# Performance work log

Measured on AMD Instinct MI355X. Metric: run time of the kernel, lower is better.

The kernel has to match this reference:

```python
import jax, jax.numpy as jnp
import numpy as np

B, S, E = 4, 2048, 1024
H = 16
HD = E // H  # head_dim = 64


def setup_inputs() -> dict:
    key = jax.random.key(0)
    ks = jax.random.split(key, 12)
    sc = 0.02
    return {
        "q_encodings": jax.random.normal(ks[0], (B, S, E), jnp.float32),
        "k_encodings": jax.random.normal(ks[1], (B, S, E), jnp.float32),
        "v_encodings": jax.random.normal(ks[2], (B, S, E), jnp.float32),
        # per-head q/k/v linear weights [H, HD, HD] and biases [H, HD]
        "Wq": jax.random.normal(ks[3], (H, HD, HD), jnp.float32) * sc,
        "bq": jax.random.normal(ks[4], (H, HD), jnp.float32) * sc,
        "Wk": jax.random.normal(ks[5], (H, HD, HD), jnp.float32) * sc,
        "bk": jax.random.normal(ks[6], (H, HD), jnp.float32) * sc,
        "Wv": jax.random.normal(ks[7], (H, HD, HD), jnp.float32) * sc,
        "bv": jax.random.normal(ks[8], (H, HD), jnp.float32) * sc,
        # output projection [E, E] + bias [E]
        "Wp": jax.random.normal(ks[9], (E, E), jnp.float32) * sc,
        "bp": jax.random.normal(ks[10], (E,), jnp.float32) * sc,
        "mask": 1,
    }


def reference(q_encodings, k_encodings, v_encodings, Wq, bq, Wk, bk, Wv, bv, Wp, bp, mask):
    b, s, e = q_encodings.shape
    h, hd, _ = Wq.shape
    split = lambda x: x.reshape(b, s, h, hd)  # per-head slices of n_embd
    # batched per-head linear projections (original loops over heads)
    Q = jnp.einsum('bshd,hde->bshe', split(q_encodings), Wq) + bq
    K = jnp.einsum('bshd,hde->bshe', split(k_encodings), Wk) + bk
    V = jnp.einsum('bshd,hde->bshe', split(v_encodings), Wv) + bv
    # scaled dot-product scores [B,H,S,S]; scale uses head_dim (Attention.n_embd)
    scores = jnp.einsum('bqhd,bkhd->bhqk', Q, K) / jnp.sqrt(jnp.float32(hd))
    if mask:  # static Python flag, matches torch `if mask:`
        causal = jnp.tril(jnp.ones((s, s), jnp.float32))
        scores = scores + jnp.where(causal == 0, jnp.float32(-jnp.inf), jnp.float32(0.0))
    attn = jax.nn.softmax(scores, axis=-1)
    ctx = jnp.einsum('bhqk,bkhd->bqhd', attn, V).reshape(b, s, e)
    return ctx @ Wp + bp
```

## Files before the change

kernel.cpp:

```cpp
#include <hip/hip_runtime.h>
#include <hip/hip_bf16.h>
#include <math.h>

typedef __bf16 bf16;
typedef __bf16 bf16x8 __attribute__((ext_vector_type(8)));
typedef float f32x4 __attribute__((ext_vector_type(4)));
typedef unsigned int u32x2 __attribute__((ext_vector_type(2)));

constexpr int B = 4, S = 2048, E = 1024, H = 16, HD = 64;

constexpr float QSCALE = 0.125f * 1.44269504088896340736f;
constexpr float DTHR = 11.5f;

static __device__ __forceinline__ float exp2_fast(float x) {
#if __has_builtin(__builtin_amdgcn_exp2f)
    return __builtin_amdgcn_exp2f(x);
#else
    float r; asm("v_exp_f32 %0, %1" : "=v"(r) : "v"(x)); return r;
#endif
}

static __device__ __forceinline__ unsigned pk_bf16(float a, float b) {
    union { bf16 h[2]; unsigned u; } r;
    r.h[0] = (bf16)a; r.h[1] = (bf16)b;
    return r.u;
}

static __device__ __forceinline__ void gl16(const void* g, void* l) {
    __builtin_amdgcn_global_load_lds(
        (__attribute__((address_space(1))) void*)g,
        (__attribute__((address_space(3))) void*)l,
        16, 0, 0);
}

__global__ __launch_bounds__(256) void prep_weights(
    const float* __restrict__ Wq, const float* __restrict__ Wk,
    const float* __restrict__ Wv, const float* __restrict__ Wp,
    bf16* __restrict__ Wt, bf16* __restrict__ Wpt)
{
    __shared__ float t[64][65];
    const int tid = threadIdx.x;
    const int x = blockIdx.x, y = blockIdx.y;
    if (y < 3) {
        const int h = x, p = y;
        const float* W = (p == 0) ? Wq : (p == 1) ? Wk : Wv;
        const float scale = (p == 0) ? QSCALE : 1.0f;
        #pragma unroll
        for (int i = 0; i < 16; ++i) {
            int idx = tid + i * 256;
            int d = idx >> 6, e = idx & 63;
            t[d][e] = W[(size_t)h * 4096 + d * 64 + e];
        }
        __syncthreads();
        bf16* dst = Wt + ((size_t)p * H + h) * 4096;
        #pragma unroll
        for (int i = 0; i < 16; ++i) {
            int idx = tid + i * 256;
            int e = idx >> 6, d = idx & 63;
            dst[e * 64 + d] = (bf16)(t[d][e] * scale);
        }
    } else {
        const int k0 = (y - 3) * 64, n0 = x * 64;
        #pragma unroll
        for (int i = 0; i < 16; ++i) {
            int idx = tid + i * 256;
            int r = idx >> 6, c = idx & 63;
            t[r][c] = Wp[(size_t)(k0 + r) * E + n0 + c];
        }
        __syncthreads();
        #pragma unroll
        for (int i = 0; i < 16; ++i) {
            int idx = tid + i * 256;
            int r = idx >> 6, c = idx & 63;
            Wpt[(size_t)(n0 + r) * E + k0 + c] = (bf16)t[c][r];
        }
    }
}

__global__ __launch_bounds__(256) void qkv_proj(
    const float* __restrict__ xq, const float* __restrict__ xk, const float* __restrict__ xv,
    const bf16* __restrict__ Wt,
    const float* __restrict__ bq, const float* __restrict__ bk, const float* __restrict__ bv,
    bf16* __restrict__ Qb, bf16* __restrict__ Kb, bf16* __restrict__ Vt)
{
    const int b = blockIdx.z, h = blockIdx.y, s0 = blockIdx.x * 128;
    const int tid = threadIdx.x;
    const int w = tid >> 6, l = tid & 63;
    const int l16 = l & 15, lg = l >> 4;
    const size_t bh = (size_t)b * H + h;

    __shared__ __align__(16) bf16 xs[128][64];
    __shared__ __align__(16) bf16 Wl[64][64];
    __shared__ __align__(16) bf16 ts[10240];

    for (int p = 0; p < 3; ++p) {
        const float* x    = (p == 0) ? xq : (p == 1) ? xk : xv;
        const float* bias = (p == 0) ? bq : (p == 1) ? bk : bv;
        const float  bsc  = (p == 0) ? QSCALE : 1.0f;

        __syncthreads();
        #pragma unroll
        for (int i = 0; i < 4; ++i) {
            int idx = tid + i * 256;
            int r = idx >> 3, g = idx & 7;
            const float* src = &x[((size_t)b * S + s0 + r) * E + h * 64 + g * 8];
            float4 f0 = *(const float4*)src;
            float4 f1 = *(const float4*)(src + 4);
            union { bf16 h8[8]; uint4 u; } pk;
            pk.h8[0] = (bf16)f0.x; pk.h8[1] = (bf16)f0.y;
            pk.h8[2] = (bf16)f0.z; pk.h8[3] = (bf16)f0.w;
            pk.h8[4] = (bf16)f1.x; pk.h8[5] = (bf16)f1.y;
            pk.h8[6] = (bf16)f1.z; pk.h8[7] = (bf16)f1.w;
            *(uint4*)&xs[r][(g ^ (r & 7)) * 8] = pk.u;
        }
        const bf16* wsrc = Wt + ((size_t)p * H + h) * 4096;
        #pragma unroll
        for (int i = 0; i < 2; ++i) {
            int idx = tid + i * 256;
            int e = idx >> 3, g = idx & 7;
            *(uint4*)&Wl[e][(g ^ (e & 7)) * 8] = *(const uint4*)(wsrc + e * 64 + g * 8);
        }
        __syncthreads();

        if (p < 2) {
            float bcol[4];
            #pragma unroll
            for (int ei = 0; ei < 4; ++ei)
                bcol[ei] = bias[h * 64 + ei * 16 + l16] * bsc;
            #pragma unroll
            for (int st = 0; st < 2; ++st) {
                const int srow = w * 32 + st * 16 + l16;
                bf16x8 a0 = *(const bf16x8*)&xs[srow][((lg    ) ^ (srow & 7)) * 8];
                bf16x8 a1 = *(const bf16x8*)&xs[srow][((4 + lg) ^ (srow & 7)) * 8];
                #pragma unroll
                for (int ei = 0; ei < 4; ++ei) {
                    const int erow = ei * 16 + l16;
                    bf16x8 b0 = *(const bf16x8*)&Wl[erow][((lg    ) ^ (erow & 7)) * 8];
                    bf16x8 b1 = *(const bf16x8*)&Wl[erow][((4 + lg) ^ (erow & 7)) * 8];
                    f32x4 acc = {0.f, 0.f, 0.f, 0.f};
                    acc = __builtin_amdgcn_mfma_f32_16x16x32_bf16(a0, b0, acc, 0, 0, 0);
                    acc = __builtin_amdgcn_mfma_f32_16x16x32_bf16(a1, b1, acc, 0, 0, 0);
                    #pragma unroll
                    for (int r = 0; r < 4; ++r)
                        ts[(w * 32 + st * 16 + 4 * lg + r) * 80 + ei * 16 + l16] =
                            (bf16)(acc[r] + bcol[ei]);
                }
            }
            __syncthreads();
            bf16* out = (p == 0) ? Qb : Kb;
            #pragma unroll
            for (int i = 0; i < 4; ++i) {
                int idx = tid + i * 256;
                int r = idx >> 3, g = idx & 7;
                uint4 v = *(const uint4*)&ts[r * 80 + g * 8];
                *(uint4*)(out + (bh * S + s0 + r) * 64 + g * 8) = v;
            }
        } else {
            float brow[4];
            #pragma unroll
            for (int r = 0; r < 4; ++r)
                brow[r] = bias[h * 64 + w * 16 + 4 * lg + r];
            const int erow = w * 16 + l16;
            bf16x8 a0 = *(const bf16x8*)&Wl[erow][((lg    ) ^ (erow & 7)) * 8];
            bf16x8 a1 = *(const bf16x8*)&Wl[erow][((4 + lg) ^ (erow & 7)) * 8];
            #pragma unroll
            for (int st = 0; st < 8; ++st) {
                const int srow = st * 16 + l16;
                bf16x8 b0 = *(const bf16x8*)&xs[srow][((lg    ) ^ (srow & 7)) * 8];
                bf16x8 b1 = *(const bf16x8*)&xs[srow][((4 + lg) ^ (srow & 7)) * 8];
                f32x4 acc = {0.f, 0.f, 0.f, 0.f};
                acc = __builtin_amdgcn_mfma_f32_16x16x32_bf16(a0, b0, acc, 0, 0, 0);
                acc = __builtin_amdgcn_mfma_f32_16x16x32_bf16(a1, b1, acc, 0, 0, 0);
                #pragma unroll
                for (int r = 0; r < 4; ++r)
                    ts[(w * 16 + 4 * lg + r) * 136 + st * 16 + l16] =
                        (bf16)(acc[r] + brow[r]);
            }
            __syncthreads();
            #pragma unroll
            for (int i = 0; i < 4; ++i) {
                int idx = tid + i * 256;
                int r = idx >> 4, g = idx & 15;
                uint4 v = *(const uint4*)&ts[r * 136 + g * 8];
                *(uint4*)(Vt + (bh * 64 + r) * S + s0 + g * 8) = v;
            }
        }
    }
}

__global__ __launch_bounds__(512) void attn(
    const bf16* __restrict__ Qb, const bf16* __restrict__ Kb,
    const bf16* __restrict__ Vt, bf16* __restrict__ ctx)
{
    const int pair = blockIdx.x;
    const int bh   = blockIdx.y;
    const int b = bh >> 4, h = bh & 15;
    const int tid = threadIdx.x;
    const int w = tid >> 6;
    const int l = tid & 63;
    const int l16 = l & 15, lg = l >> 4;

    __shared__ __align__(16) bf16 Kl[2][64][64];
    __shared__ __align__(16) bf16 Vl[2][64][64];
    __shared__ __align__(16) bf16 Pl[8][16][72];

    const bf16* Qp = Qb + (size_t)bh * S * 64;
    const bf16* Kp = Kb + (size_t)bh * S * 64;
    const bf16* Vp = Vt + (size_t)bh * 64 * S;

    const int str = tid >> 3;
    const int stc = tid & 7;
    const int sws = (stc ^ (str & 7)) * 8;

    int foff0[4], foff1[4];
    #pragma unroll
    for (int s = 0; s < 4; ++s) {
        foff0[s] = (16 * s + l16) * 64 + ((lg    ) ^ (l16 & 7)) * 8;
        foff1[s] = (16 * s + l16) * 64 + ((4 + lg) ^ (l16 & 7)) * 8;
    }
    bf16* Plw = &Pl[w][0][0];
    const int pwr = l16 * 72 + 4 * lg;
    const int prd = l16 * 72 + 8 * lg;

    const bf16 one_ = (bf16)1.0f;
    const bf16x8 ones = {one_, one_, one_, one_, one_, one_, one_, one_};

    #pragma unroll 1
    for (int half = 0; half < 2; ++half) {
        const int qt   = half ? (15 - pair) : pair;
        const int qw0  = qt * 128 + w * 16;
        const int qabs = qw0 + l16;
        const int nt   = 2 * qt + 2;

        bf16x8 qf0 = *(const bf16x8*)(Qp + (size_t)qabs * 64 + lg * 8);
        bf16x8 qf1 = *(const bf16x8*)(Qp + (size_t)qabs * 64 + 32 + lg * 8);

        f32x4 o[4] = {};
        float m_run = -1e30f, l_run = 0.f;

        {
            uint4 kreg = *(const uint4*)(Kp + (size_t)str * 64 + stc * 8);
            uint4 vreg = *(const uint4*)(Vp + (size_t)str * S + stc * 8);
            *(uint4*)&Kl[0][str][sws] = kreg;
            *(uint4*)&Vl[0][str][sws] = vreg;
        }
        int cur = 0;
        for (int t = 0; t < nt; ++t) {
            __syncthreads();
            const bool pfv = (t + 1 < nt);
            uint4 kreg, vreg;
            if (pfv) {
                const int kv1 = (t + 1) * 64;
                kreg = *(const uint4*)(Kp + (size_t)(kv1 + str) * 64 + stc * 8);
                vreg = *(const uint4*)(Vp + (size_t)str * S + kv1 + stc * 8);
            }
            const int kv0 = t * 64;
            if (kv0 < qw0 + 16) {
                const bf16* Kbase = &Kl[cur][0][0];
                const bf16* Vbase = &Vl[cur][0][0];

                float p[16];
                __builtin_amdgcn_s_setprio(1);
                #pragma unroll
                for (int s = 0; s < 4; ++s) {
                    f32x4 sc = {0.f, 0.f, 0.f, 0.f};
                    bf16x8 ka = *(const bf16x8*)(Kbase + foff0[s]);
                    bf16x8 kb = *(const bf16x8*)(Kbase + foff1[s]);
                    sc = __builtin_amdgcn_mfma_f32_16x16x32_bf16(ka, qf0, sc, 0, 0, 0);
                    sc = __builtin_amdgcn_mfma_f32_16x16x32_bf16(kb, qf1, sc, 0, 0, 0);
                    p[4 * s + 0] = sc[0]; p[4 * s + 1] = sc[1];
                    p[4 * s + 2] = sc[2]; p[4 * s + 3] = sc[3];
                }
                __builtin_amdgcn_s_setprio(0);

                if (kv0 + 63 > qw0) {
                    #pragma unroll
                    for (int i = 0; i < 16; ++i) {
                        const int kvloc = 16 * (i >> 2) + 4 * lg + (i & 3);
                        if (kv0 + kvloc > qabs) p[i] = -1e30f;
                    }
                }

                float m4[4];
                #pragma unroll
                for (int j = 0; j < 4; ++j)
                    m4[j] = fmaxf(fmaxf(p[4*j], p[4*j+1]), fmaxf(p[4*j+2], p[4*j+3]));
                float mx = fmaxf(fmaxf(m4[0], m4[1]), fmaxf(m4[2], m4[3]));
                mx = fmaxf(mx, __shfl_xor(mx, 16));
                mx = fmaxf(mx, __shfl_xor(mx, 32));
                if (!__all(mx <= m_run + DTHR)) {
                    const float m_new = fmaxf(m_run, mx);
                    const float corr = exp2_fast(m_run - m_new);
                    l_run *= corr;
                    #pragma unroll
                    for (int ds = 0; ds < 4; ++ds) {
                        o[ds][0] *= corr; o[ds][1] *= corr;
                        o[ds][2] *= corr; o[ds][3] *= corr;
                    }
                    m_run = m_new;
                }
                #pragma unroll
                for (int i = 0; i < 16; ++i) p[i] = exp2_fast(p[i] - m_run);

                #pragma unroll
                for (int s = 0; s < 4; ++s) {
                    u32x2 pw;
                    pw[0] = pk_bf16(p[4 * s + 0], p[4 * s + 1]);
                    pw[1] = pk_bf16(p[4 * s + 2], p[4 * s + 3]);
                    *(u32x2*)(Plw + pwr + 16 * s) = pw;
                }
                asm volatile("s_waitcnt lgkmcnt(0)" ::: "memory");
                bf16x8 pf0 = *(const bf16x8*)(Plw + prd);
                bf16x8 pf1 = *(const bf16x8*)(Plw + prd + 32);

                __builtin_amdgcn_s_setprio(1);
                f32x4 o5 = {0.f, 0.f, 0.f, 0.f};
                o5 = __builtin_amdgcn_mfma_f32_16x16x32_bf16(ones, pf0, o5, 0, 0, 0);
                o5 = __builtin_amdgcn_mfma_f32_16x16x32_bf16(ones, pf1, o5, 0, 0, 0);
                #pragma unroll
                for (int ds = 0; ds < 4; ++ds) {
                    bf16x8 v0 = *(const bf16x8*)(Vbase + foff0[ds]);
                    bf16x8 v1 = *(const bf16x8*)(Vbase + foff1[ds]);
                    o[ds] = __builtin_amdgcn_mfma_f32_16x16x32_bf16(v0, pf0, o[ds], 0, 0, 0);
                    o[ds] = __builtin_amdgcn_mfma_f32_16x16x32_bf16(v1, pf1, o[ds], 0, 0, 0);
                }
                __builtin_amdgcn_s_setprio(0);
                l_run += o5[0];
            }
            if (pfv) {
                *(uint4*)&Kl[cur ^ 1][str][sws] = kreg;
                *(uint4*)&Vl[cur ^ 1][str][sws] = vreg;
            }
            cur ^= 1;
        }

        const float il = 1.0f / l_run;
        bf16* crow = ctx + ((size_t)b * S + qabs) * E + h * 64;
        #pragma unroll
        for (int ds = 0; ds < 4; ++ds) {
            u32x2 pw;
            pw[0] = pk_bf16(o[ds][0] * il, o[ds][1] * il);
            pw[1] = pk_bf16(o[ds][2] * il, o[ds][3] * il);
            *(u32x2*)(crow + 16 * ds + 4 * lg) = pw;
        }
    }
}

__global__ __launch_bounds__(256) void out_gemm(
    const bf16* __restrict__ A, const bf16* __restrict__ Bt,
    const float* __restrict__ bp, float* __restrict__ C)
{
    const int n0 = blockIdx.x * 128, m0 = blockIdx.y * 128;
    const int tid = threadIdx.x;
    const int w = tid >> 6, l = tid & 63;
    const int l16 = l & 15, lg = l >> 4;
    const int wm = w >> 1, wn = w & 1;

    __shared__ __align__(16) bf16 Al[128][64];
    __shared__ __align__(16) bf16 Bl[128][64];

    f32x4 acc[4][4] = {};

    const int r8 = l >> 3;
    const int chunk = ((l & 7) ^ r8) * 8;

    for (int k0 = 0; k0 < E; k0 += 64) {
        __syncthreads();
        #pragma unroll
        for (int i = 0; i < 4; ++i) {
            const int rb = 8 * w + 32 * i;
            gl16(A  + (size_t)(m0 + rb + r8) * E + k0 + chunk, &Al[rb][0]);
            gl16(Bt + (size_t)(n0 + rb + r8) * E + k0 + chunk, &Bl[rb][0]);
        }
        __syncthreads();

        #pragma unroll
        for (int ks = 0; ks < 2; ++ks) {
            bf16x8 af[4], bfr[4];
            #pragma unroll
            for (int mi = 0; mi < 4; ++mi) {
                int r = wm * 64 + mi * 16 + l16;
                af[mi] = *(const bf16x8*)&Al[r][((ks * 4 + lg) ^ (r & 7)) * 8];
            }
            #pragma unroll
            for (int ni = 0; ni < 4; ++ni) {
                int r = wn * 64 + ni * 16 + l16;
                bfr[ni] = *(const bf16x8*)&Bl[r][((ks * 4 + lg) ^ (r & 7)) * 8];
            }
            #pragma unroll
            for (int mi = 0; mi < 4; ++mi)
                #pragma unroll
                for (int ni = 0; ni < 4; ++ni)
                    acc[mi][ni] = __builtin_amdgcn_mfma_f32_16x16x32_bf16(
                        af[mi], bfr[ni], acc[mi][ni], 0, 0, 0);
        }
    }

    #pragma unroll
    for (int ni = 0; ni < 4; ++ni) {
        const int col = n0 + wn * 64 + ni * 16 + l16;
        const float bias = bp[col];
        #pragma unroll
        for (int mi = 0; mi < 4; ++mi) {
            #pragma unroll
            for (int e = 0; e < 4; ++e) {
                int row = m0 + wm * 64 + mi * 16 + 4 * lg + e;
                C[(size_t)row * E + col] = acc[mi][ni][e] + bias;
            }
        }
    }
}

extern "C" void kernel_launch(void* const* d_in, const int* in_sizes, int n_in,
                              void* d_out, int out_size, void* d_ws, size_t ws_size,
                              hipStream_t stream)
{
    const float* xq = (const float*)d_in[0];
    const float* xk = (const float*)d_in[1];
    const float* xv = (const float*)d_in[2];
    const float* Wq = (const float*)d_in[3];
    const float* bq = (const float*)d_in[4];
    const float* Wk = (const float*)d_in[5];
    const float* bk = (const float*)d_in[6];
    const float* Wv = (const float*)d_in[7];
    const float* bv = (const float*)d_in[8];
    const float* Wp = (const float*)d_in[9];
    const float* bp = (const float*)d_in[10];
    float* out = (float*)d_out;

    char* ws = (char*)d_ws;
    const size_t sz_bhse = (size_t)B * H * S * HD;
    bf16* Qb  = (bf16*)ws;  ws += sz_bhse * 2;
    bf16* Kb  = (bf16*)ws;  ws += sz_bhse * 2;
    bf16* Vtw = (bf16*)ws;  ws += sz_bhse * 2;
    bf16* ctx = (bf16*)ws;  ws += (size_t)B * S * E * 2;
    bf16* Wpt = (bf16*)ws;  ws += (size_t)E * E * 2;
    bf16* Wt3 = (bf16*)ws;  ws += (size_t)3 * H * HD * HD * 2;

    prep_weights<<<dim3(16, 19), 256, 0, stream>>>(Wq, Wk, Wv, Wp, Wt3, Wpt);
    qkv_proj<<<dim3(S / 128, H, B), 256, 0, stream>>>(xq, xk, xv, Wt3,
                                                      bq, bk, bv, Qb, Kb, Vtw);
    attn<<<dim3(8, B * H), 512, 0, stream>>>(Qb, Kb, Vtw, ctx);
    out_gemm<<<dim3(E / 128, (B * S) / 128), 256, 0, stream>>>(ctx, Wpt, bp, out);
}
```

Measured before the change: 122.7 us.

## Switch attention to 32x32x16 MFMA with 32 queries per wave, 4 waves

The attention kernel now uses 32x32x16 bf16 MFMA tiles. Each wave owns 32 query rows instead of 16, and blocks shrink from 8 to 4 waves, each thread loading two K/V rows per tile. The larger MFMA shape cuts LDS fragment reads per FLOP and removes one cross-lane shuffle in the row max. In exchange there are fewer waves per block for latency hiding, more accumulator registers per lane, and coarser causal-skip granularity.

```diff
diff --git a/kernel.cpp b/kernel.cpp
--- a/kernel.cpp
+++ b/kernel.cpp
@@ -5,6 +5,7 @@
 typedef __bf16 bf16;
 typedef __bf16 bf16x8 __attribute__((ext_vector_type(8)));
 typedef float f32x4 __attribute__((ext_vector_type(4)));
+typedef float f32x16 __attribute__((ext_vector_type(16)));
 typedef unsigned int u32x2 __attribute__((ext_vector_type(2)));
 
 constexpr int B = 4, S = 2048, E = 1024, H = 16, HD = 64;
@@ -188,7 +189,7 @@
     }
 }
 
-__global__ __launch_bounds__(512) void attn(
+__global__ __launch_bounds__(256) void attn(
     const bf16* __restrict__ Qb, const bf16* __restrict__ Kb,
     const bf16* __restrict__ Vt, bf16* __restrict__ ctx)
 {
@@ -198,11 +199,11 @@
     const int tid = threadIdx.x;
     const int w = tid >> 6;
     const int l = tid & 63;
-    const int l16 = l & 15, lg = l >> 4;
+    const int q31 = l & 31, hi = l >> 5;
 
     __shared__ __align__(16) bf16 Kl[2][64][64];
     __shared__ __align__(16) bf16 Vl[2][64][64];
-    __shared__ __align__(16) bf16 Pl[8][16][72];
+    __shared__ __align__(16) bf16 Pl[4][32][72];
 
     const bf16* Qp = Qb + (size_t)bh * S * 64;
     const bf16* Kp = Kb + (size_t)bh * S * 64;
@@ -212,15 +213,16 @@
     const int stc = tid & 7;
     const int sws = (stc ^ (str & 7)) * 8;
 
-    int foff0[4], foff1[4];
+    int foff[2][4];
     #pragma unroll
-    for (int s = 0; s < 4; ++s) {
-        foff0[s] = (16 * s + l16) * 64 + ((lg    ) ^ (l16 & 7)) * 8;
-        foff1[s] = (16 * s + l16) * 64 + ((4 + lg) ^ (l16 & 7)) * 8;
-    }
+    for (int blk = 0; blk < 2; ++blk)
+        #pragma unroll
+        for (int ki = 0; ki < 4; ++ki)
+            foff[blk][ki] = (32 * blk + q31) * 64 + (((2 * ki + hi) ^ (q31 & 7)) * 8);
+
     bf16* Plw = &Pl[w][0][0];
-    const int pwr = l16 * 72 + 4 * lg;
-    const int prd = l16 * 72 + 8 * lg;
+    const int pwrb = q31 * 72 + 4 * hi;
+    const int prdb = q31 * 72 + 8 * hi;
 
     const bf16 one_ = (bf16)1.0f;
     const bf16x8 ones = {one_, one_, one_, one_, one_, one_, one_, one_};
@@ -228,108 +230,122 @@
     #pragma unroll 1
     for (int half = 0; half < 2; ++half) {
         const int qt   = half ? (15 - pair) : pair;
-        const int qw0  = qt * 128 + w * 16;
-        const int qabs = qw0 + l16;
+        const int qw0  = qt * 128 + w * 32;
+        const int qabs = qw0 + q31;
         const int nt   = 2 * qt + 2;
 
-        bf16x8 qf0 = *(const bf16x8*)(Qp + (size_t)qabs * 64 + lg * 8);
-        bf16x8 qf1 = *(const bf16x8*)(Qp + (size_t)qabs * 64 + 32 + lg * 8);
-
-        f32x4 o[4] = {};
+        bf16x8 qf[4];
+        #pragma unroll
+        for (int ki = 0; ki < 4; ++ki)
+            qf[ki] = *(const bf16x8*)(Qp + (size_t)qabs * 64 + 16 * ki + 8 * hi);
+
+        f32x16 o0 = {}, o1 = {};
         float m_run = -1e30f, l_run = 0.f;
 
         {
-            uint4 kreg = *(const uint4*)(Kp + (size_t)str * 64 + stc * 8);
-            uint4 vreg = *(const uint4*)(Vp + (size_t)str * S + stc * 8);
-            *(uint4*)&Kl[0][str][sws] = kreg;
-            *(uint4*)&Vl[0][str][sws] = vreg;
+            #pragma unroll
+            for (int i = 0; i < 2; ++i) {
+                const int r = str + i * 32;
+                uint4 kreg = *(const uint4*)(Kp + (size_t)r * 64 + stc * 8);
+                uint4 vreg = *(const uint4*)(Vp + (size_t)r * S + stc * 8);
+                *(uint4*)&Kl[0][r][sws] = kreg;
+                *(uint4*)&Vl[0][r][sws] = vreg;
+            }
         }
         int cur = 0;
         for (int t = 0; t < nt; ++t) {
             __syncthreads();
             const bool pfv = (t + 1 < nt);
-            uint4 kreg, vreg;
+            uint4 kreg0, kreg1, vreg0, vreg1;
             if (pfv) {
                 const int kv1 = (t + 1) * 64;
-                kreg = *(const uint4*)(Kp + (size_t)(kv1 + str) * 64 + stc * 8);
-                vreg = *(const uint4*)(Vp + (size_t)str * S + kv1 + stc * 8);
+                kreg0 = *(const uint4*)(Kp + (size_t)(kv1 + str) * 64 + stc * 8);
+                kreg1 = *(const uint4*)(Kp + (size_t)(kv1 + str + 32) * 64 + stc * 8);
+                vreg0 = *(const uint4*)(Vp + (size_t)str * S + kv1 + stc * 8);
+                vreg1 = *(const uint4*)(Vp + (size_t)(str + 32) * S + kv1 + stc * 8);
             }
             const int kv0 = t * 64;
-            if (kv0 < qw0 + 16) {
+            if (kv0 < qw0 + 32) {
                 const bf16* Kbase = &Kl[cur][0][0];
                 const bf16* Vbase = &Vl[cur][0][0];
 
-                float p[16];
+                f32x16 sc0 = {}, sc1 = {};
                 __builtin_amdgcn_s_setprio(1);
                 #pragma unroll
-                for (int s = 0; s < 4; ++s) {
-                    f32x4 sc = {0.f, 0.f, 0.f, 0.f};
-                    bf16x8 ka = *(const bf16x8*)(Kbase + foff0[s]);
-                    bf16x8 kb = *(const bf16x8*)(Kbase + foff1[s]);
-                    sc = __builtin_amdgcn_mfma_f32_16x16x32_bf16(ka, qf0, sc, 0, 0, 0);
-                    sc = __builtin_amdgcn_mfma_f32_16x16x32_bf16(kb, qf1, sc, 0, 0, 0);
-                    p[4 * s + 0] = sc[0]; p[4 * s + 1] = sc[1];
-                    p[4 * s + 2] = sc[2]; p[4 * s + 3] = sc[3];
+                for (int ki = 0; ki < 4; ++ki) {
+                    bf16x8 ka = *(const bf16x8*)(Kbase + foff[0][ki]);
+                    bf16x8 kb = *(const bf16x8*)(Kbase + foff[1][ki]);
+                    sc0 = __builtin_amdgcn_mfma_f32_32x32x16_bf16(ka, qf[ki], sc0, 0, 0, 0);
+                    sc1 = __builtin_amdgcn_mfma_f32_32x32x16_bf16(kb, qf[ki], sc1, 0, 0, 0);
                 }
                 __builtin_amdgcn_s_setprio(0);
 
+                float p[32];
+                #pragma unroll
+                for (int i = 0; i < 16; ++i) { p[i] = sc0[i]; p[16 + i] = sc1[i]; }
+
                 if (kv0 + 63 > qw0) {
                     #pragma unroll
-                    for (int i = 0; i < 16; ++i) {
-                        const int kvloc = 16 * (i >> 2) + 4 * lg + (i & 3);
+                    for (int i = 0; i < 32; ++i) {
+                        const int kvloc = 32 * (i >> 4) + (i & 3) +
+                                          8 * ((i >> 2) & 3) + 4 * hi;
                         if (kv0 + kvloc > qabs) p[i] = -1e30f;
                     }
                 }
 
-                float m4[4];
-                #pragma unroll
-                for (int j = 0; j < 4; ++j)
-                    m4[j] = fmaxf(fmaxf(p[4*j], p[4*j+1]), fmaxf(p[4*j+2], p[4*j+3]));
-                float mx = fmaxf(fmaxf(m4[0], m4[1]), fmaxf(m4[2], m4[3]));
-                mx = fmaxf(mx, __shfl_xor(mx, 16));
+                float m8[8];
+                #pragma unroll
+                for (int j = 0; j < 8; ++j)
+                    m8[j] = fmaxf(fmaxf(p[4*j], p[4*j+1]), fmaxf(p[4*j+2], p[4*j+3]));
+                float mx = fmaxf(fmaxf(fmaxf(m8[0], m8[1]), fmaxf(m8[2], m8[3])),
+                                 fmaxf(fmaxf(m8[4], m8[5]), fmaxf(m8[6], m8[7])));
                 mx = fmaxf(mx, __shfl_xor(mx, 32));
                 if (!__all(mx <= m_run + DTHR)) {
                     const float m_new = fmaxf(m_run, mx);
                     const float corr = exp2_fast(m_run - m_new);
                     l_run *= corr;
                     #pragma unroll
-                    for (int ds = 0; ds < 4; ++ds) {
-                        o[ds][0] *= corr; o[ds][1] *= corr;
-                        o[ds][2] *= corr; o[ds][3] *= corr;
-                    }
+                    for (int i = 0; i < 16; ++i) { o0[i] *= corr; o1[i] *= corr; }
                     m_run = m_new;
                 }
                 #pragma unroll
-                for (int i = 0; i < 16; ++i) p[i] = exp2_fast(p[i] - m_run);
-
-                #pragma unroll
-                for (int s = 0; s < 4; ++s) {
-                    u32x2 pw;
-                    pw[0] = pk_bf16(p[4 * s + 0], p[4 * s + 1]);
-                    pw[1] = pk_bf16(p[4 * s + 2], p[4 * s + 3]);
-                    *(u32x2*)(Plw + pwr + 16 * s) = pw;
-                }
+                for (int i = 0; i < 32; ++i) p[i] = exp2_fast(p[i] - m_run);
+
+                #pragma unroll
+                for (int b2 = 0; b2 < 2; ++b2)
+                    #pragma unroll
+                    for (int g = 0; g < 4; ++g) {
+                        u32x2 pw;
+                        pw[0] = pk_bf16(p[16*b2 + 4*g + 0], p[16*b2 + 4*g + 1]);
+                        pw[1] = pk_bf16(p[16*b2 + 4*g + 2], p[16*b2 + 4*g + 3]);
+                        *(u32x2*)(Plw + pwrb + 32 * b2 + 8 * g) = pw;
+                    }
                 asm volatile("s_waitcnt lgkmcnt(0)" ::: "memory");
-                bf16x8 pf0 = *(const bf16x8*)(Plw + prd);
-                bf16x8 pf1 = *(const bf16x8*)(Plw + prd + 32);
+                bf16x8 pfr[4];
+                #pragma unroll
+                for (int ki = 0; ki < 4; ++ki)
+                    pfr[ki] = *(const bf16x8*)(Plw + prdb + 16 * ki);
 
                 __builtin_amdgcn_s_setprio(1);
-                f32x4 o5 = {0.f, 0.f, 0.f, 0.f};
-                o5 = __builtin_amdgcn_mfma_f32_16x16x32_bf16(ones, pf0, o5, 0, 0, 0);
-                o5 = __builtin_amdgcn_mfma_f32_16x16x32_bf16(ones, pf1, o5, 0, 0, 0);
-                #pragma unroll
-                for (int ds = 0; ds < 4; ++ds) {
-                    bf16x8 v0 = *(const bf16x8*)(Vbase + foff0[ds]);
-                    bf16x8 v1 = *(const bf16x8*)(Vbase + foff1[ds]);
-                    o[ds] = __builtin_amdgcn_mfma_f32_16x16x32_bf16(v0, pf0, o[ds], 0, 0, 0);
-                    o[ds] = __builtin_amdgcn_mfma_f32_16x16x32_bf16(v1, pf1, o[ds], 0, 0, 0);
+                f32x16 lac = {};
+                #pragma unroll
+                for (int ki = 0; ki < 4; ++ki)
+                    lac = __builtin_amdgcn_mfma_f32_32x32x16_bf16(ones, pfr[ki], lac, 0, 0, 0);
+                #pragma unroll
+                for (int ki = 0; ki < 4; ++ki) {
+                    bf16x8 v0 = *(const bf16x8*)(Vbase + foff[0][ki]);
+                    bf16x8 v1 = *(const bf16x8*)(Vbase + foff[1][ki]);
+                    o0 = __builtin_amdgcn_mfma_f32_32x32x16_bf16(v0, pfr[ki], o0, 0, 0, 0);
+                    o1 = __builtin_amdgcn_mfma_f32_32x32x16_bf16(v1, pfr[ki], o1, 0, 0, 0);
                 }
                 __builtin_amdgcn_s_setprio(0);
-                l_run += o5[0];
+                l_run += lac[0];
             }
             if (pfv) {
-                *(uint4*)&Kl[cur ^ 1][str][sws] = kreg;
-                *(uint4*)&Vl[cur ^ 1][str][sws] = vreg;
+                *(uint4*)&Kl[cur ^ 1][str][sws]      = kreg0;
+                *(uint4*)&Kl[cur ^ 1][str + 32][sws] = kreg1;
+                *(uint4*)&Vl[cur ^ 1][str][sws]      = vreg0;
+                *(uint4*)&Vl[cur ^ 1][str + 32][sws] = vreg1;
             }
             cur ^= 1;
         }
@@ -337,11 +353,15 @@
         const float il = 1.0f / l_run;
         bf16* crow = ctx + ((size_t)b * S + qabs) * E + h * 64;
         #pragma unroll
-        for (int ds = 0; ds < 4; ++ds) {
+        for (int g = 0; g < 4; ++g) {
             u32x2 pw;
-            pw[0] = pk_bf16(o[ds][0] * il, o[ds][1] * il);
-            pw[1] = pk_bf16(o[ds][2] * il, o[ds][3] * il);
-            *(u32x2*)(crow + 16 * ds + 4 * lg) = pw;
+            pw[0] = pk_bf16(o0[4*g + 0] * il, o0[4*g + 1] * il);
+            pw[1] = pk_bf16(o0[4*g + 2] * il, o0[4*g + 3] * il);
+            *(u32x2*)(crow + 8 * g + 4 * hi) = pw;
+            u32x2 pw1;
+            pw1[0] = pk_bf16(o1[4*g + 0] * il, o1[4*g + 1] * il);
+            pw1[1] = pk_bf16(o1[4*g + 2] * il, o1[4*g + 3] * il);
+            *(u32x2*)(crow + 32 + 8 * g + 4 * hi) = pw1;
         }
     }
 }
@@ -440,6 +460,6 @@
     prep_weights<<<dim3(16, 19), 256, 0, stream>>>(Wq, Wk, Wv, Wp, Wt3, Wpt);
     qkv_proj<<<dim3(S / 128, H, B), 256, 0, stream>>>(xq, xk, xv, Wt3,
                                                       bq, bk, bv, Qb, Kb, Vtw);
-    attn<<<dim3(8, B * H), 512, 0, stream>>>(Qb, Kb, Vtw, ctx);
+    attn<<<dim3(8, B * H), 256, 0, stream>>>(Qb, Kb, Vtw, ctx);
     out_gemm<<<dim3(E / 128, (B * S) / 128), 256, 0, stream>>>(ctx, Wpt, bp, out);
 }
```

New measurement: 133.9 us. 9.1% more time.
